# Optimization experiments

Measured on AMD Instinct MI355X. Metric: run time of the kernel, lower is better.

## Reference

```python
import jax, jax.numpy as jnp
import numpy as np

N, K, D = 50000, 16, 128
EPS = 1e-5

def _linear_params(key, fan_in, shape_w, shape_b):
    k1, k2 = jax.random.split(key)
    s = 1.0 / np.sqrt(fan_in)
    W = jax.random.uniform(k1, shape_w, minval=-s, maxval=s, dtype=jnp.float32)
    b = jax.random.uniform(k2, shape_b, minval=-s, maxval=s, dtype=jnp.float32)
    return W, b

def setup_inputs() -> dict:
    key = jax.random.key(0)
    ks = jax.random.split(key, 9)
    Wh, bh = _linear_params(ks[0], D, (D, D), (D,))
    Wt, bt = _linear_params(ks[1], D, (D, D), (D,))
    W1, b1 = _linear_params(ks[2], D, (D, D), (D,))
    W2, b2 = _linear_params(ks[3], D, (D, D), (D,))
    return {
        "x": jax.random.normal(ks[4], (N, D), dtype=jnp.float32),
        "e_h_input": jax.random.normal(ks[5], (N, D), dtype=jnp.float32),
        "e_t_input": jax.random.normal(ks[6], (N, D), dtype=jnp.float32),
        "topk_indices": jax.random.randint(ks[7], (N, K), 0, N),
        "topk_weights": jax.random.uniform(ks[8], (N, K), dtype=jnp.float32),
        "Wh": Wh, "bh": bh, "Wt": Wt, "bt": bt,
        "W1": W1, "b1": b1, "W2": W2, "b2": b2,
        "gamma": jnp.ones((D,), jnp.float32),
        "beta": jnp.zeros((D,), jnp.float32),
    }

def reference(x, e_h_input, e_t_input, topk_indices, topk_weights,
              Wh, bh, Wt, bt, W1, b1, W2, b2, gamma, beta):
    e_h = e_h_input @ Wh.T + bh            # [N, D]
    e_t = e_t_input @ Wt.T + bt            # [N, D]
    Nb_h = e_t[topk_indices]               # [N, K, D] neighbor gather
    p = topk_weights[..., None]            # [N, K, 1]
    e_h_exp = e_h[:, None, :]              # [N, 1, D]
    eh_r = p * Nb_h + (1.0 - p) * e_h_exp  # gated mix
    gate = jnp.tanh(e_h_exp + eh_r)
    ka_prob = jax.nn.softmax(jnp.sum(Nb_h * gate, axis=-1), axis=-1)  # [N, K]
    e_Nh = jnp.einsum('nk,nkd->nd', ka_prob, Nb_h)                    # [N, D]
    sum_emb = jax.nn.leaky_relu((x + e_Nh) @ W1.T + b1, 0.01)
    bi_emb = jax.nn.leaky_relu((x * e_Nh) @ W2.T + b2, 0.01)
    h = sum_emb + bi_emb                   # dropout is identity in eval
    mu = jnp.mean(h, axis=-1, keepdims=True)
    var = jnp.var(h, axis=-1, keepdims=True)
    return (h - mu) / jnp.sqrt(var + EPS) * gamma + beta
```

## Files before the change

### kernel.cpp

```cpp
#include <hip/hip_runtime.h>
#include <stdint.h>

#define NROWS 50000
#define KNB 16
#define DD 128
#define LN_EPS 1e-5f

typedef unsigned short ushort_t;
using frag_ab = __attribute__((ext_vector_type(8))) short;
using frag_cd = __attribute__((ext_vector_type(4))) float;

static __device__ __forceinline__ float bf2f(uint32_t u) {
    union { uint32_t i; float f; } v; v.i = u << 16; return v.f;
}
static __device__ __forceinline__ ushort_t f2bf(float f) {
    union { float f; uint32_t i; } v; v.f = f;
    uint32_t x = v.i;
    return (ushort_t)((x + 0x7fffu + ((x >> 16) & 1u)) >> 16);
}
static __device__ __forceinline__ uint32_t packbf(float a, float b) {
    return (uint32_t)f2bf(a) | ((uint32_t)f2bf(b) << 16);
}
static __device__ __forceinline__ float leaky(float v) {
    return v > 0.0f ? v : 0.01f * v;
}
static __device__ __forceinline__ float tanh_fast(float z) {
    float e = __expf(2.0f * z);
    return 1.0f - 2.0f / (e + 1.0f);
}
static __device__ __forceinline__ void split_bf(float f, ushort_t& hi, ushort_t& lo) {
    hi = f2bf(f);
    lo = f2bf(f - bf2f(hi));
}
static __device__ __forceinline__ uint32_t cvtpk(float lo, float hi) {
    uint32_t r;
    asm("v_cvt_pk_bf16_f32 %0, %1, %2" : "=v"(r) : "v"(lo), "v"(hi));
    return r;
}
static __device__ __forceinline__ frag_ab load_wfrag(const float* wp) {
    float4 u = *(const float4*)(wp);
    float4 v = *(const float4*)(wp + 4);
    union { uint32_t d[4]; frag_ab f; } r;
    r.d[0] = cvtpk(u.x, u.y);
    r.d[1] = cvtpk(u.z, u.w);
    r.d[2] = cvtpk(v.x, v.y);
    r.d[3] = cvtpk(v.z, v.w);
    return r.f;
}

__global__ __launch_bounds__(256) void linear_mfma2(
    const float* __restrict__ inA, const float* __restrict__ WA,
    const float* __restrict__ bA, float* __restrict__ outA,
    const float* __restrict__ inB, const float* __restrict__ WB,
    const float* __restrict__ bB, float* __restrict__ outB, int nblk)
{
    const int which = blockIdx.x >= nblk;
    const int bid   = which ? blockIdx.x - nblk : blockIdx.x;
    const float* in   = which ? inB : inA;
    const float* W    = which ? WB  : WA;
    const float* bias = which ? bB  : bA;
    float* out        = which ? outB : outA;

    __shared__ ushort_t Wl[128 * 136];
    const int tid = threadIdx.x;
    for (int i = tid; i < 128 * 64; i += 256) {
        int row = i >> 6, cp = (i & 63) << 1;
        float2 w = *(const float2*)(W + row * 128 + cp);
        *(uint32_t*)(&Wl[row * 136 + cp]) = packbf(w.x, w.y);
    }
    const int wv = tid >> 6, lane = tid & 63;
    const int quad = lane >> 4, lq = lane & 15;
    float bn[8];
    #pragma unroll
    for (int nt = 0; nt < 8; ++nt) bn[nt] = bias[nt * 16 + lq];
    __syncthreads();

    const int r0 = bid * 64 + wv * 16;
    const int arow = r0 + lq;
    const int arc = arow < NROWS ? arow : NROWS - 1;

    frag_ab Ahi[4], Alo[4];
    const float* ip = in + (size_t)arc * DD + quad * 8;
    #pragma unroll
    for (int c = 0; c < 4; ++c) {
        float4 u = *(const float4*)(ip + c * 32);
        float4 v = *(const float4*)(ip + c * 32 + 4);
        float uu[8] = {u.x, u.y, u.z, u.w, v.x, v.y, v.z, v.w};
        #pragma unroll
        for (int i = 0; i < 8; ++i) {
            ushort_t h, l; split_bf(uu[i], h, l);
            Ahi[c][i] = (short)h; Alo[c][i] = (short)l;
        }
    }

    #pragma unroll
    for (int nt = 0; nt < 8; ++nt) {
        frag_cd acc = {0.f, 0.f, 0.f, 0.f};
        #pragma unroll
        for (int c = 0; c < 4; ++c) {
            frag_ab B = *(const frag_ab*)(&Wl[(nt * 16 + lq) * 136 + c * 32 + quad * 8]);
            acc = __builtin_amdgcn_mfma_f32_16x16x32_bf16(Alo[c], B, acc, 0, 0, 0);
            acc = __builtin_amdgcn_mfma_f32_16x16x32_bf16(Ahi[c], B, acc, 0, 0, 0);
        }
        #pragma unroll
        for (int r = 0; r < 4; ++r) {
            int orow = r0 + quad * 4 + r;
            if (orow < NROWS)
                out[(size_t)orow * DD + nt * 16 + lq] = acc[r] + bn[nt];
        }
    }
}

__global__ __launch_bounds__(256, 4) void mega_kernel(
    const float* e_h, const float* __restrict__ e_t,
    const int* __restrict__ topk_idx, const float* __restrict__ topk_w,
    const float* __restrict__ x,
    const float* W1, const float* __restrict__ b1,
    const float* W2, const float* __restrict__ b2,
    const float* __restrict__ gamma, const float* __restrict__ beta,
    float* out, int niters)
{
    __shared__ ushort_t aHi[16][136], aLo[16][136];
    __shared__ ushort_t mHi[16][136], mLo[16][136];
    __shared__ float hL[16][132];

    const int tid  = threadIdx.x;
    const int wv   = tid >> 6;
    const int lane = tid & 63;
    const int quad = lane >> 4, lq = lane & 15;
    const int n0   = wv * 32;

    float b1v[2], b2v[2];
    #pragma unroll
    for (int t = 0; t < 2; ++t) {
        b1v[t] = b1[n0 + t * 16 + lq];
        b2v[t] = b2[n0 + t * 16 + lq];
    }
    const float g0 = gamma[lane], g1 = gamma[lane + 64];
    const float be0 = beta[lane], be1 = beta[lane + 64];

    const float* w1p = W1 + (size_t)(n0 + lq) * DD + quad * 8;
    const float* w2p = W2 + (size_t)(n0 + lq) * DD + quad * 8;

    for (int c = blockIdx.x; c < niters; c += gridDim.x) {
        const int r0 = c << 4;

        #pragma unroll
        for (int q = 0; q < 4; ++q) {
            const int lr = 4 * wv + q;
            const int nu = __builtin_amdgcn_readfirstlane(r0 + lr);
            int   tk[KNB];
            float pk[KNB];
            #pragma unroll
            for (int k = 0; k < KNB; ++k) tk[k] = topk_idx[nu * KNB + k];
            #pragma unroll
            for (int k = 0; k < KNB; ++k) pk[k] = topk_w[nu * KNB + k];
            float2 nb[KNB];
            #pragma unroll
            for (int k = 0; k < KNB; ++k) {
                int t = tk[k];
                t = ((unsigned)t < (unsigned)NROWS) ? t : 0;
                nb[k] = *(const float2*)(e_t + (size_t)t * DD + 2 * lane);
            }
            const float2 ehv = *(const float2*)(e_h + (size_t)nu * DD + 2 * lane);
            const float2 xv  = *(const float2*)(x   + (size_t)nu * DD + 2 * lane);

            const float e2x = ehv.x + ehv.x, e2y = ehv.y + ehv.y;

            float s[KNB];
            #pragma unroll
            for (int k = 0; k < KNB; ++k) {
                const float p = pk[k];
                const float ax = __builtin_fmaf(p, nb[k].x - ehv.x, e2x);
                const float ay = __builtin_fmaf(p, nb[k].y - ehv.y, e2y);
                float part = nb[k].x * tanh_fast(ax)
                           + nb[k].y * tanh_fast(ay);
                #pragma unroll
                for (int off = 32; off >= 1; off >>= 1)
                    part += __shfl_xor(part, off, 64);
                s[k] = part;
            }
            float mx = s[0];
            #pragma unroll
            for (int k = 1; k < KNB; ++k) mx = fmaxf(mx, s[k]);
            float sum = 0.0f;
            #pragma unroll
            for (int k = 0; k < KNB; ++k) { s[k] = __expf(s[k] - mx); sum += s[k]; }
            const float inv = 1.0f / sum;
            float e0 = 0.0f, e1 = 0.0f;
            #pragma unroll
            for (int k = 0; k < KNB; ++k) { e0 += s[k] * nb[k].x; e1 += s[k] * nb[k].y; }
            e0 *= inv; e1 *= inv;

            const float a0 = xv.x + e0, a1 = xv.y + e1;
            const float m0 = xv.x * e0, m1 = xv.y * e1;
            ushort_t h0, l0, h1, l1;
            split_bf(a0, h0, l0); split_bf(a1, h1, l1);
            *(uint32_t*)(&aHi[lr][2 * lane]) = (uint32_t)h0 | ((uint32_t)h1 << 16);
            *(uint32_t*)(&aLo[lr][2 * lane]) = (uint32_t)l0 | ((uint32_t)l1 << 16);
            split_bf(m0, h0, l0); split_bf(m1, h1, l1);
            *(uint32_t*)(&mHi[lr][2 * lane]) = (uint32_t)h0 | ((uint32_t)h1 << 16);
            *(uint32_t*)(&mLo[lr][2 * lane]) = (uint32_t)l0 | ((uint32_t)l1 << 16);
        }
        __syncthreads();

        {
            frag_cd aA0 = {0.f,0.f,0.f,0.f}, aA1 = {0.f,0.f,0.f,0.f};
            frag_cd aM0 = {0.f,0.f,0.f,0.f}, aM1 = {0.f,0.f,0.f,0.f};
            #pragma unroll
            for (int kc = 0; kc < 4; ++kc) {
                frag_ab B10 = load_wfrag(w1p + kc * 32);
                frag_ab B11 = load_wfrag(w1p + 16 * DD + kc * 32);
                frag_ab B20 = load_wfrag(w2p + kc * 32);
                frag_ab B21 = load_wfrag(w2p + 16 * DD + kc * 32);
                frag_ab Ah = *(const frag_ab*)(&aHi[lq][kc * 32 + quad * 8]);
                frag_ab Al = *(const frag_ab*)(&aLo[lq][kc * 32 + quad * 8]);
                frag_ab Mh = *(const frag_ab*)(&mHi[lq][kc * 32 + quad * 8]);
                frag_ab Ml = *(const frag_ab*)(&mLo[lq][kc * 32 + quad * 8]);
                aA0 = __builtin_amdgcn_mfma_f32_16x16x32_bf16(Al, B10, aA0, 0, 0, 0);
                aA0 = __builtin_amdgcn_mfma_f32_16x16x32_bf16(Ah, B10, aA0, 0, 0, 0);
                aA1 = __builtin_amdgcn_mfma_f32_16x16x32_bf16(Al, B11, aA1, 0, 0, 0);
                aA1 = __builtin_amdgcn_mfma_f32_16x16x32_bf16(Ah, B11, aA1, 0, 0, 0);
                aM0 = __builtin_amdgcn_mfma_f32_16x16x32_bf16(Ml, B20, aM0, 0, 0, 0);
                aM0 = __builtin_amdgcn_mfma_f32_16x16x32_bf16(Mh, B20, aM0, 0, 0, 0);
                aM1 = __builtin_amdgcn_mfma_f32_16x16x32_bf16(Ml, B21, aM1, 0, 0, 0);
                aM1 = __builtin_amdgcn_mfma_f32_16x16x32_bf16(Mh, B21, aM1, 0, 0, 0);
            }
            #pragma unroll
            for (int r = 0; r < 4; ++r) {
                const int row = quad * 4 + r;
                hL[row][n0 + lq]      = leaky(aA0[r] + b1v[0]) + leaky(aM0[r] + b2v[0]);
                hL[row][n0 + 16 + lq] = leaky(aA1[r] + b1v[1]) + leaky(aM1[r] + b2v[1]);
            }
        }
        __syncthreads();

        #pragma unroll
        for (int q = 0; q < 4; ++q) {
            const int lr = 4 * wv + q;
            const float h0 = hL[lr][lane], h1 = hL[lr][lane + 64];
            float s = h0 + h1, qq = h0 * h0 + h1 * h1;
            #pragma unroll
            for (int off = 32; off >= 1; off >>= 1) {
                s  += __shfl_xor(s,  off, 64);
                qq += __shfl_xor(qq, off, 64);
            }
            const float mu  = s * (1.0f / DD);
            const float var = qq * (1.0f / DD) - mu * mu;
            const float rs  = rsqrtf(var + LN_EPS);
            out[(size_t)(r0 + lr) * DD + lane]      = (h0 - mu) * rs * g0 + be0;
            out[(size_t)(r0 + lr) * DD + lane + 64] = (h1 - mu) * rs * g1 + be1;
        }
        __syncthreads();
    }
}

extern "C" void kernel_launch(void* const* d_in, const int* in_sizes, int n_in,
                              void* d_out, int out_size, void* d_ws, size_t ws_size,
                              hipStream_t stream) {
    const float* x      = (const float*)d_in[0];
    const float* ehi    = (const float*)d_in[1];
    const float* eti    = (const float*)d_in[2];
    const int*   tidx   = (const int*)d_in[3];
    const float* tw     = (const float*)d_in[4];
    const float* Wh     = (const float*)d_in[5];
    const float* bh     = (const float*)d_in[6];
    const float* Wt     = (const float*)d_in[7];
    const float* bt     = (const float*)d_in[8];
    const float* W1     = (const float*)d_in[9];
    const float* b1     = (const float*)d_in[10];
    const float* W2     = (const float*)d_in[11];
    const float* b2     = (const float*)d_in[12];
    const float* gamma  = (const float*)d_in[13];
    const float* beta   = (const float*)d_in[14];

    float* e_h = (float*)d_out;
    float* e_t = (float*)d_ws;

    const int nblk = (NROWS + 63) / 64;

    linear_mfma2<<<2 * nblk, 256, 0, stream>>>(ehi, Wh, bh, e_h,
                                               eti, Wt, bt, e_t, nblk);
    mega_kernel<<<1024, 256, 0, stream>>>(e_h, e_t, tidx, tw, x,
                                          W1, b1, W2, b2, gamma, beta,
                                          (float*)d_out, NROWS / 16);
}
```

Measured before the change: 269.8 us.

## Keep weight fragments in registers and grid-stride the linear projection kernel

The projection kernel stops staging the full weight matrix in shared memory for every 64-row block. Each wave now keeps a 32-column slice of the weights as bf16 MFMA fragments in registers and loops over 16-row tiles with a persistent grid of 2048 blocks. This removes the per-block weight conversion and LDS traffic, at the cost of each 16-row input tile being loaded and split by four waves instead of one. The fused mega kernel's grid also grows from 1024 to 1536 blocks.

```diff
diff --git a/kernel.cpp b/kernel.cpp
--- a/kernel.cpp
+++ b/kernel.cpp
@@ -17,9 +17,6 @@
     union { float f; uint32_t i; } v; v.f = f;
     uint32_t x = v.i;
     return (ushort_t)((x + 0x7fffu + ((x >> 16) & 1u)) >> 16);
-}
-static __device__ __forceinline__ uint32_t packbf(float a, float b) {
-    return (uint32_t)f2bf(a) | ((uint32_t)f2bf(b) << 16);
 }
 static __device__ __forceinline__ float leaky(float v) {
     return v > 0.0f ? v : 0.01f * v;
@@ -48,65 +45,64 @@
     return r.f;
 }
 
-__global__ __launch_bounds__(256) void linear_mfma2(
+__global__ __launch_bounds__(256, 4) void linear_stream(
     const float* __restrict__ inA, const float* __restrict__ WA,
     const float* __restrict__ bA, float* __restrict__ outA,
     const float* __restrict__ inB, const float* __restrict__ WB,
-    const float* __restrict__ bB, float* __restrict__ outB, int nblk)
+    const float* __restrict__ bB, float* __restrict__ outB, int half)
 {
-    const int which = blockIdx.x >= nblk;
-    const int bid   = which ? blockIdx.x - nblk : blockIdx.x;
+    const int which = blockIdx.x >= half;
+    const int bid   = which ? blockIdx.x - half : blockIdx.x;
     const float* in   = which ? inB : inA;
     const float* W    = which ? WB  : WA;
     const float* bias = which ? bB  : bA;
     float* out        = which ? outB : outA;
 
-    __shared__ ushort_t Wl[128 * 136];
-    const int tid = threadIdx.x;
-    for (int i = tid; i < 128 * 64; i += 256) {
-        int row = i >> 6, cp = (i & 63) << 1;
-        float2 w = *(const float2*)(W + row * 128 + cp);
-        *(uint32_t*)(&Wl[row * 136 + cp]) = packbf(w.x, w.y);
-    }
-    const int wv = tid >> 6, lane = tid & 63;
+    const int tid  = threadIdx.x;
+    const int wv   = tid >> 6;
+    const int lane = tid & 63;
     const int quad = lane >> 4, lq = lane & 15;
-    float bn[8];
+    const int n0   = wv * 32;
+
+    frag_ab BW[2][4];
     #pragma unroll
-    for (int nt = 0; nt < 8; ++nt) bn[nt] = bias[nt * 16 + lq];
-    __syncthreads();
-
-    const int r0 = bid * 64 + wv * 16;
-    const int arow = r0 + lq;
-    const int arc = arow < NROWS ? arow : NROWS - 1;
-
-    frag_ab Ahi[4], Alo[4];
-    const float* ip = in + (size_t)arc * DD + quad * 8;
+    for (int t = 0; t < 2; ++t) {
+        const float* wr = W + (size_t)(n0 + t * 16 + lq) * DD + quad * 8;
+        #pragma unroll
+        for (int kc = 0; kc < 4; ++kc)
+            BW[t][kc] = load_wfrag(wr + kc * 32);
+    }
+    float bn[2];
     #pragma unroll
-    for (int c = 0; c < 4; ++c) {
-        float4 u = *(const float4*)(ip + c * 32);
-        float4 v = *(const float4*)(ip + c * 32 + 4);
-        float uu[8] = {u.x, u.y, u.z, u.w, v.x, v.y, v.z, v.w};
-        #pragma unroll
-        for (int i = 0; i < 8; ++i) {
-            ushort_t h, l; split_bf(uu[i], h, l);
-            Ahi[c][i] = (short)h; Alo[c][i] = (short)l;
-        }
-    }
-
-    #pragma unroll
-    for (int nt = 0; nt < 8; ++nt) {
-        frag_cd acc = {0.f, 0.f, 0.f, 0.f};
-        #pragma unroll
-        for (int c = 0; c < 4; ++c) {
-            frag_ab B = *(const frag_ab*)(&Wl[(nt * 16 + lq) * 136 + c * 32 + quad * 8]);
-            acc = __builtin_amdgcn_mfma_f32_16x16x32_bf16(Alo[c], B, acc, 0, 0, 0);
-            acc = __builtin_amdgcn_mfma_f32_16x16x32_bf16(Ahi[c], B, acc, 0, 0, 0);
-        }
-        #pragma unroll
-        for (int r = 0; r < 4; ++r) {
-            int orow = r0 + quad * 4 + r;
-            if (orow < NROWS)
-                out[(size_t)orow * DD + nt * 16 + lq] = acc[r] + bn[nt];
+    for (int t = 0; t < 2; ++t) bn[t] = bias[n0 + t * 16 + lq];
+
+    const int ntiles = NROWS / 16;
+    for (int t0 = bid; t0 < ntiles; t0 += half) {
+        const int r0 = t0 * 16;
+        frag_ab Ahi[4], Alo[4];
+        const float* ip = in + (size_t)(r0 + lq) * DD + quad * 8;
+        #pragma unroll
+        for (int kc = 0; kc < 4; ++kc) {
+            float4 u = *(const float4*)(ip + kc * 32);
+            float4 v = *(const float4*)(ip + kc * 32 + 4);
+            float uu[8] = {u.x, u.y, u.z, u.w, v.x, v.y, v.z, v.w};
+            #pragma unroll
+            for (int i = 0; i < 8; ++i) {
+                ushort_t h, l; split_bf(uu[i], h, l);
+                Ahi[kc][i] = (short)h; Alo[kc][i] = (short)l;
+            }
+        }
+        #pragma unroll
+        for (int t = 0; t < 2; ++t) {
+            frag_cd acc = {0.f, 0.f, 0.f, 0.f};
+            #pragma unroll
+            for (int kc = 0; kc < 4; ++kc) {
+                acc = __builtin_amdgcn_mfma_f32_16x16x32_bf16(Alo[kc], BW[t][kc], acc, 0, 0, 0);
+                acc = __builtin_amdgcn_mfma_f32_16x16x32_bf16(Ahi[kc], BW[t][kc], acc, 0, 0, 0);
+            }
+            #pragma unroll
+            for (int r = 0; r < 4; ++r)
+                out[(size_t)(r0 + quad * 4 + r) * DD + n0 + t * 16 + lq] = acc[r] + bn[t];
         }
     }
 }
@@ -277,11 +273,10 @@
     float* e_h = (float*)d_out;
     float* e_t = (float*)d_ws;
 
-    const int nblk = (NROWS + 63) / 64;
-
-    linear_mfma2<<<2 * nblk, 256, 0, stream>>>(ehi, Wh, bh, e_h,
-                                               eti, Wt, bt, e_t, nblk);
-    mega_kernel<<<1024, 256, 0, stream>>>(e_h, e_t, tidx, tw, x,
+    const int half = 1024;
+    linear_stream<<<2 * half, 256, 0, stream>>>(ehi, Wh, bh, e_h,
+                                                eti, Wt, bt, e_t, half);
+    mega_kernel<<<1536, 256, 0, stream>>>(e_h, e_t, tidx, tw, x,
                                           W1, b1, W2, b2, gamma, beta,
                                           (float*)d_out, NROWS / 16);
 }
```

After: 306.6 us. 13.7% more time.
